# Optimization experiments

Hardware: AMD Instinct MI355X
Metric: run time of the kernel (lower is better)

The kernel has to match this reference:

```python
import math
import jax, jax.numpy as jnp
import numpy as np

B, T_IN, R = 32, 24, 512
T_HIST, WIDTH, MODES, NLAYERS = 24, 128, 64, 4
IN_CH = T_HIST + 4
STEPS = 12
DT = 1.0


def setup_inputs() -> dict:
    key = jax.random.key(0)
    ks = jax.random.split(key, 12)
    scale = 1.0 / math.sqrt(WIDTH * WIDTH)
    return {
        "z": jax.random.normal(ks[0], (B, T_IN, R), dtype=jnp.float32),
        "t_grid": jax.random.uniform(ks[1], (B, T_IN), dtype=jnp.float32) * 100.0,
        "fc0_w": jax.random.normal(ks[2], (IN_CH, WIDTH), dtype=jnp.float32) / math.sqrt(IN_CH),
        "fc0_b": jax.random.normal(ks[3], (WIDTH,), dtype=jnp.float32) * 0.01,
        "spec_wr": jax.random.normal(ks[4], (NLAYERS, WIDTH, WIDTH, MODES), dtype=jnp.float32) * scale,
        "spec_wi": jax.random.normal(ks[5], (NLAYERS, WIDTH, WIDTH, MODES), dtype=jnp.float32) * scale,
        "conv_w": jax.random.normal(ks[6], (NLAYERS, WIDTH, WIDTH), dtype=jnp.float32) / math.sqrt(WIDTH),
        "conv_b": jax.random.normal(ks[7], (NLAYERS, WIDTH), dtype=jnp.float32) * 0.01,
        "fc1_w": jax.random.normal(ks[8], (WIDTH, 2 * WIDTH), dtype=jnp.float32) / math.sqrt(WIDTH),
        "fc1_b": jax.random.normal(ks[9], (2 * WIDTH,), dtype=jnp.float32) * 0.01,
        "fc2_w": jax.random.normal(ks[10], (2 * WIDTH, 1), dtype=jnp.float32) / math.sqrt(2 * WIDTH),
        "fc2_b": jax.random.normal(ks[11], (1,), dtype=jnp.float32) * 0.01,
        "steps": STEPS,
    }


def _fno_block(h, w_cplx, cw, cb, r):
    # h: (B, W, R). Spectral conv: rfft -> truncated complex mul -> irfft.
    x_ft = jnp.fft.rfft(h, axis=-1)                      # (B, W, R//2+1) complex
    m = w_cplx.shape[-1]                                  # modes (<= R//2+1)
    out_m = jnp.einsum('bim,iom->bom', x_ft[:, :, :m], w_cplx)
    out_ft = jnp.pad(out_m, ((0, 0), (0, 0), (0, x_ft.shape[-1] - m)))
    spec = jnp.fft.irfft(out_ft, n=r, axis=-1)
    # 1x1 conv (pointwise over channels) + bias
    pw = jnp.einsum('oi,bir->bor', cw, h) + cb[None, :, None]
    return jax.nn.gelu(spec + pw, approximate=False)


def reference(z, t_grid, fc0_w, fc0_b, spec_wr, spec_wi, conv_w, conv_b,
              fc1_w, fc1_b, fc2_w, fc2_b, steps):
    b, _, r = z.shape
    t_hist = fc0_w.shape[0] - 4
    seq0 = z[:, -t_hist:]                 # (B, t_hist, R)
    t_start = t_grid[:, -1]               # (B,)
    x_coord = jnp.linspace(0.0, 1.0, r, dtype=z.dtype)  # (R,)
    spec_w = spec_wr + 1j * spec_wi       # (L, W, W, M) complex
    nlayers = conv_w.shape[0]

    def step(seq, i):
        tt = t_start + (i + 1).astype(z.dtype) * DT      # (B,)
        ang24 = 2.0 * math.pi * tt / 24.0
        ang168 = 2.0 * math.pi * tt / 168.0
        tf = jnp.stack([
            jnp.broadcast_to(jnp.sin(ang24)[:, None], (b, r)),
            jnp.broadcast_to(jnp.cos(ang24)[:, None], (b, r)),
            jnp.broadcast_to(jnp.sin(ang168)[:, None], (b, r)),
            jnp.broadcast_to(x_coord[None, :], (b, r)),
        ], axis=-1)                                       # (B, R, 4)
        h = jnp.concatenate([jnp.swapaxes(seq, 1, 2), tf], axis=-1)  # (B, R, t_hist+4)
        h = h @ fc0_w + fc0_b                             # (B, R, W)
        h = jnp.swapaxes(h, 1, 2)                         # (B, W, R)
        for l in range(nlayers):
            h = _fno_block(h, spec_w[l], conv_w[l], conv_b[l], r)
        h = jnp.swapaxes(h, 1, 2)                         # (B, R, W)
        h = jax.nn.gelu(h @ fc1_w + fc1_b, approximate=False)
        dx = (h @ fc2_w + fc2_b)[..., 0]                  # (B, R)
        z_next = seq[:, -1, :] + dx
        new_seq = jnp.concatenate([seq[:, 1:], z_next[:, None]], axis=1)
        return new_seq, z_next

    _, preds = jax.lax.scan(step, seq0, jnp.arange(steps))
    return jnp.swapaxes(preds, 0, 1)                      # (B, steps, R)
```

## Files before the change

### kernel.cpp

```cpp
#include <hip/hip_runtime.h>
#include <math.h>


#define NB 32
#define NR 512
#define NW 128
#define NM 64
#define NTH 24
#define NLAY 4
#define NSTEPS 12
#define SEQROWS 36

typedef unsigned short u16;
typedef unsigned int u32;
typedef __attribute__((ext_vector_type(8))) short bf16x8;
typedef __attribute__((ext_vector_type(4))) float f32x4;
#define MFMA16(a, b, c) __builtin_amdgcn_mfma_f32_16x16x32_bf16((a), (b), (c), 0, 0, 0)

__device__ __forceinline__ float gelu_exact(float x) {
    return 0.5f * x * (1.0f + erff(x * 0.70710678118654752f));
}
__device__ __forceinline__ float bf2f(u16 u) {
    union { u32 i; float f; } v; v.i = ((u32)u) << 16; return v.f;
}
__device__ __forceinline__ u16 f2bf_hi(float x) {
    union { float f; u32 i; } v; v.f = x; return (u16)(v.i >> 16);
}
__device__ __forceinline__ u16 f2bf_lo(float x) {
    float h = bf2f(f2bf_hi(x));
    return f2bf_hi(x - h);
}
__device__ __forceinline__ bf16x8 negbf(bf16x8 a) {
#pragma unroll
    for (int i = 0; i < 8; i++) a[i] ^= (short)0x8000;
    return a;
}

__global__ void build_tables_planes(u16* __restrict__ f1, u16* __restrict__ f2,
                                    u16* __restrict__ gt1, u16* __restrict__ gt2) {
    int idx = blockIdx.x * 256 + threadIdx.x;
    int mc = idx >> 9, r = idx & 511, m = mc & 63;
    int p = (m * r) & 511;
    float a = (float)p * (1.0f / 256.0f);
    float c = cospif(a), s = sinpif(a);
    float Fv = (mc < 64) ? c : -s;
    float cm = (m == 0) ? (1.0f / 512.0f) : (2.0f / 512.0f);
    float Gv = (mc < 64) ? cm * c : ((m == 0) ? 0.0f : -cm * s);
    f1[idx] = f2bf_hi(Fv); f2[idx] = f2bf_lo(Fv);
    size_t g = (size_t)r * 128 + mc;
    gt1[g] = f2bf_hi(Gv); gt2[g] = f2bf_lo(Gv);
}

__global__ __launch_bounds__(256) void prep_specw(const float* __restrict__ wr, const float* __restrict__ wi,
                           u16* __restrict__ wr1, u16* __restrict__ wr2,
                           u16* __restrict__ wi1, u16* __restrict__ wi2) {
    __shared__ float tile[128][65];
    int l = blockIdx.x >> 7, o = blockIdx.x & 127;
    int tid = threadIdx.x;
    size_t sbase = (size_t)l * 1048576 + (size_t)o * 64;
    size_t dbase = (size_t)l * 64 * 16384 + (size_t)o * 128;
    for (int pass = 0; pass < 2; pass++) {
        const float* src = pass ? wi : wr;
        u16* d1 = pass ? wi1 : wr1;
        u16* d2 = pass ? wi2 : wr2;
        if (pass) __syncthreads();
        for (int e = tid; e < 8192; e += 256) {
            int i = e >> 6, m = e & 63;
            tile[i][m] = src[sbase + (size_t)i * 8192 + m];
        }
        __syncthreads();
        for (int e = tid; e < 4096; e += 256) {
            int m = e >> 6, i2 = (e & 63) * 2;
            float v0 = tile[i2][m], v1 = tile[i2 + 1][m];
            u32 hh = (u32)f2bf_hi(v0) | ((u32)f2bf_hi(v1) << 16);
            u32 ll = (u32)f2bf_lo(v0) | ((u32)f2bf_lo(v1) << 16);
            size_t d = dbase + (size_t)m * 16384 + i2;
            *(u32*)&d1[d] = hh;
            *(u32*)&d2[d] = ll;
        }
    }
}

__global__ void prep_cw(const float* __restrict__ cw, u16* __restrict__ c1, u16* __restrict__ c2) {
    int idx = blockIdx.x * 256 + threadIdx.x;
    float v = cw[idx];
    c1[idx] = f2bf_hi(v); c2[idx] = f2bf_lo(v);
}

__global__ void prep_fc1t(const float* __restrict__ fc1_w,
                          u16* __restrict__ f11, u16* __restrict__ f12) {
    int idx = blockIdx.x * 256 + threadIdx.x;
    int j = idx >> 7, c = idx & 127;
    float v = fc1_w[(size_t)c * 256 + j];
    f11[idx] = f2bf_hi(v); f12[idx] = f2bf_lo(v);
}

__global__ void init_seq_kernel(const float* __restrict__ z, float* __restrict__ seq) {
    int idx = blockIdx.x * 256 + threadIdx.x;
    int b = idx / (NTH * NR);
    int rem = idx - b * (NTH * NR);
    seq[(size_t)b * SEQROWS * NR + rem] = z[idx];
}

__global__ __launch_bounds__(256) void fc0_kernel(const float* __restrict__ seq,
        const float* __restrict__ t_grid, const float* __restrict__ fc0_w,
        const float* __restrict__ fc0_b, u16* __restrict__ ht1, u16* __restrict__ ht2,
        u16* __restrict__ htc1, u16* __restrict__ htc2, int step) {
    __shared__ float wlds[28 * 128];
    __shared__ float blds[128];
    int b = blockIdx.y, rblk = blockIdx.x;
    int tid = threadIdx.x;
    for (int t = tid; t < 28 * 128; t += 256) wlds[t] = fc0_w[t];
    if (tid < 128) blds[tid] = fc0_b[tid];
    __syncthreads();
    int lane = tid & 63, wq = tid >> 6;
    int r = rblk * 64 + lane;
    float sv[24];
    const float* sp = seq + ((size_t)b * SEQROWS + step) * NR + r;
#pragma unroll
    for (int t = 0; t < 24; t++) sv[t] = sp[(size_t)t * NR];
    float tt = t_grid[b * 24 + 23] + (float)(step + 1);
    float ang24 = 6.28318530717958647692f * tt * (1.0f / 24.0f);
    float ang168 = 6.28318530717958647692f * tt * (1.0f / 168.0f);
    float s24 = sinf(ang24), c24 = cosf(ang24), s168 = sinf(ang168);
    float xc = (float)r * (1.0f / 511.0f);
    size_t rowoff = ((size_t)b * NR + r) * NW;
#pragma unroll 2
    for (int w0 = 0; w0 < 32; w0 += 2) {
        float acc2[2];
#pragma unroll
        for (int q = 0; q < 2; q++) {
            int w = wq * 32 + w0 + q;
            float acc = blds[w];
#pragma unroll
            for (int t = 0; t < 24; t++) acc += sv[t] * wlds[t * 128 + w];
            acc += s24 * wlds[24 * 128 + w] + c24 * wlds[25 * 128 + w]
                 + s168 * wlds[26 * 128 + w] + xc * wlds[27 * 128 + w];
            acc2[q] = acc;
        }
        u16 h0 = f2bf_hi(acc2[0]), h1 = f2bf_hi(acc2[1]);
        u16 l0 = f2bf_lo(acc2[0]), l1 = f2bf_lo(acc2[1]);
        size_t off = rowoff + wq * 32 + w0;
        *(u32*)&ht1[off] = (u32)h0 | ((u32)h1 << 16);
        *(u32*)&ht2[off] = (u32)l0 | ((u32)l1 << 16);
        int w = wq * 32 + w0;
        size_t coff = ((size_t)b * 128 + w) * 512 + r;
        htc1[coff] = h0; htc1[coff + 512] = h1;
        htc2[coff] = l0; htc2[coff + 512] = l1;
    }
}

__global__ __launch_bounds__(256) void dft_mfma(const u16* __restrict__ f1, const u16* __restrict__ f2,
        const u16* __restrict__ htc1, const u16* __restrict__ htc2,
        u16* __restrict__ x1, u16* __restrict__ x2) {
    __shared__ __align__(16) u16 A1[2][1280], A2[2][1280];
    __shared__ __align__(16) u16 B1[2][2560], B2[2][2560];
    int bx = blockIdx.x;
    int b = bx >> 1, ch = bx & 1;
    int mct = blockIdx.y * 32;
    int tid = threadIdx.x, wid = tid >> 6, l = tid & 63;
    int wm0 = (wid >> 1) * 16, wn0 = (wid & 1) * 32;
    int arow = (l & 15), kgrp = (l >> 4) * 8;
    f32x4 acc0 = {0.f, 0.f, 0.f, 0.f}, acc1 = {0.f, 0.f, 0.f, 0.f};
    int pa_pl = tid >> 7, pa_row = (tid >> 2) & 31, pa_seg = tid & 3;
    const u16* asrc = (pa_pl ? f2 : f1) + (size_t)(mct + pa_row) * 512 + pa_seg * 8;
    int aoff = pa_row * 40 + pa_seg * 8;
    int b_row = (tid >> 2) & 63, b_seg = tid & 3;
    const u16* bsrc1 = htc1 + ((size_t)b * 128 + ch * 64 + b_row) * 512 + b_seg * 8;
    const u16* bsrc2 = htc2 + ((size_t)b * 128 + ch * 64 + b_row) * 512 + b_seg * 8;
    int boff = b_row * 40 + b_seg * 8;
    uint4 raO, rbO0, rbO1, raE, rbE0, rbE1;
    raO = *(const uint4*)(asrc); rbO0 = *(const uint4*)(bsrc1); rbO1 = *(const uint4*)(bsrc2);
    *(uint4*)((pa_pl ? A2[0] : A1[0]) + aoff) = raO;
    *(uint4*)(B1[0] + boff) = rbO0;
    *(uint4*)(B2[0] + boff) = rbO1;
    raO = *(const uint4*)(asrc + 32); rbO0 = *(const uint4*)(bsrc1 + 32); rbO1 = *(const uint4*)(bsrc2 + 32);
    raE = *(const uint4*)(asrc + 64); rbE0 = *(const uint4*)(bsrc1 + 64); rbE1 = *(const uint4*)(bsrc2 + 64);
    __syncthreads();
#define DFT_COMPUTE(BUF)                                                       \
    {   bf16x8 a1 = *(const bf16x8*)&A1[BUF][(wm0 + arow) * 40 + kgrp];        \
        bf16x8 a2 = *(const bf16x8*)&A2[BUF][(wm0 + arow) * 40 + kgrp];        \
        bf16x8 b10 = *(const bf16x8*)&B1[BUF][(wn0 + arow) * 40 + kgrp];       \
        bf16x8 b20 = *(const bf16x8*)&B2[BUF][(wn0 + arow) * 40 + kgrp];       \
        bf16x8 b11 = *(const bf16x8*)&B1[BUF][(wn0 + 16 + arow) * 40 + kgrp];  \
        bf16x8 b21 = *(const bf16x8*)&B2[BUF][(wn0 + 16 + arow) * 40 + kgrp];  \
        acc0 = MFMA16(a1, b10, acc0);                                          \
        acc0 = MFMA16(a1, b20, acc0);                                          \
        acc0 = MFMA16(a2, b10, acc0);                                          \
        acc1 = MFMA16(a1, b11, acc1);                                          \
        acc1 = MFMA16(a1, b21, acc1);                                          \
        acc1 = MFMA16(a2, b11, acc1); }
    for (int k = 0; k < 16; k += 2) {
        DFT_COMPUTE(0)
        *(uint4*)((pa_pl ? A2[1] : A1[1]) + aoff) = raO;
        *(uint4*)(B1[1] + boff) = rbO0;
        *(uint4*)(B2[1] + boff) = rbO1;
        if (k < 13) {
            int ko = (k + 3) * 32;
            raO = *(const uint4*)(asrc + ko); rbO0 = *(const uint4*)(bsrc1 + ko); rbO1 = *(const uint4*)(bsrc2 + ko);
        }
        __syncthreads();
        DFT_COMPUTE(1)
        if (k < 14) {
            *(uint4*)((pa_pl ? A2[0] : A1[0]) + aoff) = raE;
            *(uint4*)(B1[0] + boff) = rbE0;
            *(uint4*)(B2[0] + boff) = rbE1;
            if (k < 12) {
                int ko = (k + 4) * 32;
                raE = *(const uint4*)(asrc + ko); rbE0 = *(const uint4*)(bsrc1 + ko); rbE1 = *(const uint4*)(bsrc2 + ko);
            }
        }
        __syncthreads();
    }
#undef DFT_COMPUTE
    int mcr = mct + wm0 + (l >> 4) * 4;
    int n0 = bx * 64 + wn0 + (l & 15);
#pragma unroll
    for (int j = 0; j < 4; j++) {
        size_t o0 = (size_t)(mcr + j) * 4096 + n0;
        x1[o0] = f2bf_hi(acc0[j]); x2[o0] = f2bf_lo(acc0[j]);
        size_t o1 = o0 + 16;
        x1[o1] = f2bf_hi(acc1[j]); x2[o1] = f2bf_lo(acc1[j]);
    }
}

__global__ __launch_bounds__(256) void modemix_mfma(const u16* __restrict__ x1, const u16* __restrict__ x2,
        const u16* __restrict__ wr1, const u16* __restrict__ wr2,
        const u16* __restrict__ wi1, const u16* __restrict__ wi2,
        u16* __restrict__ y1, u16* __restrict__ y2, int layer) {
    __shared__ __align__(16) u16 WR1[2][1280], WR2[2][1280], WI1[2][1280], WI2[2][1280];
    __shared__ __align__(16) u16 XR1[2][1280], XR2[2][1280], XI1[2][1280], XI2[2][1280];
    int m = blockIdx.x, oq = blockIdx.y;
    int tid = threadIdx.x, wid = tid >> 6, l = tid & 63;
    int wo0 = (wid >> 1) * 16, wb0 = (wid & 1) * 16;
    int arow = (l & 15), kgrp = (l >> 4) * 8;
    f32x4 ar = {0.f, 0.f, 0.f, 0.f}, ai = {0.f, 0.f, 0.f, 0.f};
    size_t wbase = (((size_t)layer * 64 + m) * 128 + oq * 32) * 128;
    int s0 = tid >> 7, srow = (tid >> 2) & 31, sseg = tid & 3;
    const u16* wsrc0 = (s0 ? wr2 : wr1) + wbase + (size_t)srow * 128 + sseg * 8;
    const u16* wsrc1 = (s0 ? wi2 : wi1) + wbase + (size_t)srow * 128 + sseg * 8;
    const u16* xb = s0 ? x2 : x1;
    const u16* xsrc0 = xb + (size_t)m * 4096 + srow * 128 + sseg * 8;
    const u16* xsrc1 = xb + (size_t)(64 + m) * 4096 + srow * 128 + sseg * 8;
    int soff = srow * 40 + sseg * 8;
    u16* wd0_0 = (s0 ? WR2[0] : WR1[0]) + soff;  u16* wd0_1 = (s0 ? WR2[1] : WR1[1]) + soff;
    u16* wd1_0 = (s0 ? WI2[0] : WI1[0]) + soff;  u16* wd1_1 = (s0 ? WI2[1] : WI1[1]) + soff;
    u16* xd0_0 = (s0 ? XR2[0] : XR1[0]) + soff;  u16* xd0_1 = (s0 ? XR2[1] : XR1[1]) + soff;
    u16* xd1_0 = (s0 ? XI2[0] : XI1[0]) + soff;  u16* xd1_1 = (s0 ? XI2[1] : XI1[1]) + soff;
    uint4 rwO0, rwO1, rxO0, rxO1, rwE0, rwE1, rxE0, rxE1;
    rwO0 = *(const uint4*)(wsrc0); rwO1 = *(const uint4*)(wsrc1);
    rxO0 = *(const uint4*)(xsrc0); rxO1 = *(const uint4*)(xsrc1);
    *(uint4*)wd0_0 = rwO0; *(uint4*)wd1_0 = rwO1;
    *(uint4*)xd0_0 = rxO0; *(uint4*)xd1_0 = rxO1;
    rwO0 = *(const uint4*)(wsrc0 + 32); rwO1 = *(const uint4*)(wsrc1 + 32);
    rxO0 = *(const uint4*)(xsrc0 + 32); rxO1 = *(const uint4*)(xsrc1 + 32);
    rwE0 = *(const uint4*)(wsrc0 + 64); rwE1 = *(const uint4*)(wsrc1 + 64);
    rxE0 = *(const uint4*)(xsrc0 + 64); rxE1 = *(const uint4*)(xsrc1 + 64);
    __syncthreads();
#define MM_COMPUTE(BUF)                                                        \
    {   int ao = (wo0 + arow) * 40 + kgrp;                                     \
        int bo = (wb0 + arow) * 40 + kgrp;                                     \
        bf16x8 Wr1 = *(const bf16x8*)&WR1[BUF][ao], Wr2 = *(const bf16x8*)&WR2[BUF][ao]; \
        bf16x8 Wi1 = *(const bf16x8*)&WI1[BUF][ao], Wi2 = *(const bf16x8*)&WI2[BUF][ao]; \
        bf16x8 Xr1 = *(const bf16x8*)&XR1[BUF][bo], Xr2 = *(const bf16x8*)&XR2[BUF][bo]; \
        bf16x8 Xi1 = *(const bf16x8*)&XI1[BUF][bo], Xi2 = *(const bf16x8*)&XI2[BUF][bo]; \
        bf16x8 nWi1 = negbf(Wi1), nWi2 = negbf(Wi2);                           \
        ar = MFMA16(Wr1, Xr1, ar); ar = MFMA16(Wr1, Xr2, ar); ar = MFMA16(Wr2, Xr1, ar); \
        ar = MFMA16(nWi1, Xi1, ar); ar = MFMA16(nWi1, Xi2, ar); ar = MFMA16(nWi2, Xi1, ar); \
        ai = MFMA16(Wi1, Xr1, ai); ai = MFMA16(Wi1, Xr2, ai); ai = MFMA16(Wi2, Xr1, ai); \
        ai = MFMA16(Wr1, Xi1, ai); ai = MFMA16(Wr1, Xi2, ai); ai = MFMA16(Wr2, Xi1, ai); }
    for (int k = 0; k < 4; k += 2) {
        MM_COMPUTE(0)
        *(uint4*)wd0_1 = rwO0; *(uint4*)wd1_1 = rwO1;
        *(uint4*)xd0_1 = rxO0; *(uint4*)xd1_1 = rxO1;
        if (k == 0) {
            rwO0 = *(const uint4*)(wsrc0 + 96); rwO1 = *(const uint4*)(wsrc1 + 96);
            rxO0 = *(const uint4*)(xsrc0 + 96); rxO1 = *(const uint4*)(xsrc1 + 96);
        }
        __syncthreads();
        MM_COMPUTE(1)
        if (k == 0) {
            *(uint4*)wd0_0 = rwE0; *(uint4*)wd1_0 = rwE1;
            *(uint4*)xd0_0 = rxE0; *(uint4*)xd1_0 = rxE1;
        }
        __syncthreads();
    }
#undef MM_COMPUTE
    int ob = oq * 32 + wo0 + (l >> 4) * 4;
    int bb = wb0 + (l & 15);
#pragma unroll
    for (int j = 0; j < 4; j++) {
        size_t o = ((size_t)bb * 128 + ob + j) * 128;
        y1[o + m] = f2bf_hi(ar[j]); y2[o + m] = f2bf_lo(ar[j]);
        y1[o + 64 + m] = f2bf_hi(ai[j]); y2[o + 64 + m] = f2bf_lo(ai[j]);
    }
}

__global__ __launch_bounds__(256) void idft_conv_mfma(const u16* __restrict__ y1, const u16* __restrict__ y2,
        const u16* __restrict__ gt1, const u16* __restrict__ gt2,
        const u16* __restrict__ hc1, const u16* __restrict__ hc2,
        const u16* __restrict__ cw1, const u16* __restrict__ cw2,
        const float* __restrict__ conv_b,
        u16* __restrict__ hn1, u16* __restrict__ hn2,
        u16* __restrict__ htc1, u16* __restrict__ htc2, int layer, int wtr) {
    __shared__ __align__(16) u16 A1[2][2560], A2[2][2560];
    __shared__ __align__(16) u16 B1[2][2560], B2[2][2560];
    __shared__ __align__(16) u16 T1[64 * 66], T2[64 * 66];
    int rt = blockIdx.x * 64, ot = blockIdx.y * 64, b = blockIdx.z;
    int tid = threadIdx.x, wid = tid >> 6, l = tid & 63;
    int wo0 = (wid >> 1) * 32, wr0 = (wid & 1) * 32;
    int arow = (l & 15), kgrp = (l >> 4) * 8;
    int srow = (tid >> 2) & 63, sseg = tid & 3;
    int soff = srow * 40 + sseg * 8;
    const u16* ya = y1 + ((size_t)b * 128 + ot + srow) * 128 + sseg * 8;
    const u16* yb = y2 + ((size_t)b * 128 + ot + srow) * 128 + sseg * 8;
    const u16* ca = cw1 + ((size_t)layer * 128 + ot + srow) * 128 + sseg * 8;
    const u16* cb = cw2 + ((size_t)layer * 128 + ot + srow) * 128 + sseg * 8;
    const u16* ga = gt1 + (size_t)(rt + srow) * 128 + sseg * 8;
    const u16* gb = gt2 + (size_t)(rt + srow) * 128 + sseg * 8;
    const u16* ha = hc1 + ((size_t)b * 512 + rt + srow) * 128 + sseg * 8;
    const u16* hb = hc2 + ((size_t)b * 512 + rt + srow) * 128 + sseg * 8;
    f32x4 acc[2][2] = {{{0.f,0.f,0.f,0.f},{0.f,0.f,0.f,0.f}},{{0.f,0.f,0.f,0.f},{0.f,0.f,0.f,0.f}}};
    uint4 raO0, raO1, rbO0, rbO1, raE0, raE1, rbE0, rbE1;
#define IDFT_LOAD(chk, Ra0, Ra1, Rb0, Rb1)                                    \
    {   int k0_ = ((chk) & 3) * 32;                                           \
        if ((chk) < 4) {                                                      \
            Ra0 = *(const uint4*)(ya + k0_); Ra1 = *(const uint4*)(yb + k0_); \
            Rb0 = *(const uint4*)(ga + k0_); Rb1 = *(const uint4*)(gb + k0_); \
        } else {                                                              \
            Ra0 = *(const uint4*)(ca + k0_); Ra1 = *(const uint4*)(cb + k0_); \
            Rb0 = *(const uint4*)(ha + k0_); Rb1 = *(const uint4*)(hb + k0_); \
        } }
#define IDFT_STORE(BUF, Ra0, Ra1, Rb0, Rb1)                                   \
    {   *(uint4*)(A1[BUF] + soff) = Ra0; *(uint4*)(A2[BUF] + soff) = Ra1;     \
        *(uint4*)(B1[BUF] + soff) = Rb0; *(uint4*)(B2[BUF] + soff) = Rb1; }
#define IDFT_COMPUTE(BUF)                                                     \
    {   bf16x8 bfr[2][2];                                                     \
        _Pragma("unroll")                                                     \
        for (int rf = 0; rf < 2; rf++) {                                      \
            bfr[rf][0] = *(const bf16x8*)&B1[BUF][(wr0 + rf * 16 + arow) * 40 + kgrp]; \
            bfr[rf][1] = *(const bf16x8*)&B2[BUF][(wr0 + rf * 16 + arow) * 40 + kgrp]; \
        }                                                                     \
        _Pragma("unroll")                                                     \
        for (int of = 0; of < 2; of++) {                                      \
            bf16x8 a1 = *(const bf16x8*)&A1[BUF][(wo0 + of * 16 + arow) * 40 + kgrp]; \
            bf16x8 a2 = *(const bf16x8*)&A2[BUF][(wo0 + of * 16 + arow) * 40 + kgrp]; \
            _Pragma("unroll")                                                 \
            for (int rf = 0; rf < 2; rf++) {                                  \
                acc[of][rf] = MFMA16(a1, bfr[rf][0], acc[of][rf]);            \
                acc[of][rf] = MFMA16(a1, bfr[rf][1], acc[of][rf]);            \
                acc[of][rf] = MFMA16(a2, bfr[rf][0], acc[of][rf]);            \
            }                                                                 \
        } }
    IDFT_LOAD(0, raO0, raO1, rbO0, rbO1)
    IDFT_STORE(0, raO0, raO1, rbO0, rbO1)
    IDFT_LOAD(1, raO0, raO1, rbO0, rbO1)
    IDFT_LOAD(2, raE0, raE1, rbE0, rbE1)
    __syncthreads();
    for (int k = 0; k < 8; k += 2) {
        IDFT_COMPUTE(0)
        IDFT_STORE(1, raO0, raO1, rbO0, rbO1)
        if (k < 5) IDFT_LOAD(k + 3, raO0, raO1, rbO0, rbO1)
        __syncthreads();
        IDFT_COMPUTE(1)
        if (k < 6) {
            IDFT_STORE(0, raE0, raE1, rbE0, rbE1)
            if (k < 4) IDFT_LOAD(k + 4, raE0, raE1, rbE0, rbE1)
        }
        __syncthreads();
    }
#undef IDFT_LOAD
#undef IDFT_STORE
#undef IDFT_COMPUTE
#pragma unroll
    for (int of = 0; of < 2; of++) {
        int obl = wo0 + of * 16 + (l >> 4) * 4;
        int ob = ot + obl;
#pragma unroll
        for (int rf = 0; rf < 2; rf++) {
            int rloc = wr0 + rf * 16 + (l & 15);
            int r = rt + rloc;
            float v0 = gelu_exact(acc[of][rf][0] + conv_b[layer * 128 + ob + 0]);
            float v1 = gelu_exact(acc[of][rf][1] + conv_b[layer * 128 + ob + 1]);
            float v2 = gelu_exact(acc[of][rf][2] + conv_b[layer * 128 + ob + 2]);
            float v3 = gelu_exact(acc[of][rf][3] + conv_b[layer * 128 + ob + 3]);
            ushort4 hv, lv;
            hv.x = f2bf_hi(v0); hv.y = f2bf_hi(v1); hv.z = f2bf_hi(v2); hv.w = f2bf_hi(v3);
            lv.x = f2bf_lo(v0); lv.y = f2bf_lo(v1); lv.z = f2bf_lo(v2); lv.w = f2bf_lo(v3);
            size_t off = ((size_t)b * 512 + r) * 128 + ob;
            *(ushort4*)&hn1[off] = hv;
            *(ushort4*)&hn2[off] = lv;
            if (wtr) {
                T1[(obl + 0) * 66 + rloc] = hv.x; T1[(obl + 1) * 66 + rloc] = hv.y;
                T1[(obl + 2) * 66 + rloc] = hv.z; T1[(obl + 3) * 66 + rloc] = hv.w;
                T2[(obl + 0) * 66 + rloc] = lv.x; T2[(obl + 1) * 66 + rloc] = lv.y;
                T2[(obl + 2) * 66 + rloc] = lv.z; T2[(obl + 3) * 66 + rloc] = lv.w;
            }
        }
    }
    if (wtr) {
        __syncthreads();
#pragma unroll
        for (int q = 0; q < 8; q++) {
            int t = tid + q * 256;
            int o = t >> 5, ru = t & 31;
            u32 vh = *(const u32*)&T1[o * 66 + ru * 2];
            u32 vl = *(const u32*)&T2[o * 66 + ru * 2];
            size_t off = ((size_t)b * 128 + ot + o) * 512 + rt + ru * 2;
            *(u32*)&htc1[off] = vh;
            *(u32*)&htc2[off] = vl;
        }
    }
}

__global__ __launch_bounds__(256) void head_mfma(const u16* __restrict__ ht1, const u16* __restrict__ ht2,
        const u16* __restrict__ f11, const u16* __restrict__ f12,
        const float* __restrict__ fc1_b, const float* __restrict__ fc2_w,
        const float* __restrict__ fc2_b,
        const float* __restrict__ t_grid, const float* __restrict__ fc0_w,
        const float* __restrict__ fc0_b,
        float* __restrict__ seq, float* __restrict__ preds,
        u16* __restrict__ nht1, u16* __restrict__ nht2,
        u16* __restrict__ nhtc1, u16* __restrict__ nhtc2,
        int step, int do_fc0) {
    __shared__ __align__(16) u16 POOL[25600];
    __shared__ float fc2s[256], fc1bs[256];
    u16* HA1 = POOL;
    u16* HA2 = POOL + 10240;
    u16* HB1 = POOL + 20480;
    u16* HB2 = POOL + 23040;
    int blk = blockIdx.x;
    int b = blk >> 3, r0 = (blk & 7) * 64;
    int tid = threadIdx.x, wid = tid >> 6, l = tid & 63;
    fc2s[tid] = fc2_w[tid];
    fc1bs[tid] = fc1_b[tid];
    int arow = l & 15, kgrp = (l >> 4) * 8;
    f32x4 acc[16];
#pragma unroll
    for (int jf = 0; jf < 16; jf++) acc[jf] = (f32x4){0.f, 0.f, 0.f, 0.f};
    for (int k0 = 0; k0 < 128; k0 += 32) {
        __syncthreads();
#pragma unroll
        for (int q = 0; q < 8; q++) {
            int t = tid + q * 256;
            int pl = t >> 10, j = (t >> 2) & 255, seg = t & 3;
            const u16* src = (pl ? f12 : f11) + (size_t)j * 128 + k0 + seg * 8;
            *(uint4*)((pl ? HA2 : HA1) + j * 40 + seg * 8) = *(const uint4*)src;
        }
#pragma unroll
        for (int q = 0; q < 2; q++) {
            int t = tid + q * 256;
            int pl = t >> 8, rr = (t >> 2) & 63, seg = t & 3;
            const u16* src = (pl ? ht2 : ht1) + ((size_t)b * 512 + r0 + rr) * 128 + k0 + seg * 8;
            *(uint4*)((pl ? HB2 : HB1) + rr * 40 + seg * 8) = *(const uint4*)src;
        }
        __syncthreads();
        int bo = (wid * 16 + arow) * 40 + kgrp;
        bf16x8 b1 = *(const bf16x8*)&HB1[bo];
        bf16x8 b2 = *(const bf16x8*)&HB2[bo];
#pragma unroll
        for (int jf = 0; jf < 16; jf++) {
            int ao = (jf * 16 + arow) * 40 + kgrp;
            bf16x8 a1 = *(const bf16x8*)&HA1[ao];
            bf16x8 a2 = *(const bf16x8*)&HA2[ao];
            acc[jf] = MFMA16(a1, b1, acc[jf]);
            acc[jf] = MFMA16(a1, b2, acc[jf]);
            acc[jf] = MFMA16(a2, b1, acc[jf]);
        }
    }
    __syncthreads();
    float dx = 0.0f;
#pragma unroll
    for (int jf = 0; jf < 16; jf++) {
        int jbase = jf * 16 + (l >> 4) * 4;
#pragma unroll
        for (int jj = 0; jj < 4; jj++) {
            int j = jbase + jj;
            dx += gelu_exact(acc[jf][jj] + fc1bs[j]) * fc2s[j];
        }
    }
    dx += __shfl_xor(dx, 16);
    dx += __shfl_xor(dx, 32);
    bool zlane = ((l >> 4) == 0);
    int rml = wid * 16 + arow;
    float zn = 0.0f;
    if (zlane) {
        int r = r0 + rml;
        zn = seq[((size_t)b * SEQROWS + step + 23) * NR + r] + dx + fc2_b[0];
        seq[((size_t)b * SEQROWS + step + 24) * NR + r] = zn;
        preds[((size_t)b * NSTEPS + step) * NR + r] = zn;
    }
    if (!do_fc0) return;
    float* win = (float*)POOL;
    float* wl  = (float*)POOL + 2048;
    float* bl  = (float*)POOL + 2048 + 3584;
    for (int t = tid; t < 23 * 64; t += 256) {
        int tr = t >> 6, c = t & 63;
        win[tr * 64 + c] = seq[((size_t)b * SEQROWS + step + 1 + tr) * NR + r0 + c];
    }
    for (int t = tid; t < 28 * 128; t += 256) wl[t] = fc0_w[t];
    if (tid < 128) bl[tid] = fc0_b[tid];
    if (zlane) win[23 * 64 + rml] = zn;
    __syncthreads();
    int lane = tid & 63, wq = tid >> 6;
    int r = r0 + lane;
    float sv[24];
#pragma unroll
    for (int t = 0; t < 24; t++) sv[t] = win[t * 64 + lane];
    float tt = t_grid[b * 24 + 23] + (float)(step + 2);
    float ang24 = 6.28318530717958647692f * tt * (1.0f / 24.0f);
    float ang168 = 6.28318530717958647692f * tt * (1.0f / 168.0f);
    float s24 = sinf(ang24), c24 = cosf(ang24), s168 = sinf(ang168);
    float xc = (float)r * (1.0f / 511.0f);
    size_t rowoff = ((size_t)b * NR + r) * NW;
#pragma unroll 2
    for (int w0 = 0; w0 < 32; w0 += 2) {
        float acc2[2];
#pragma unroll
        for (int q = 0; q < 2; q++) {
            int w = wq * 32 + w0 + q;
            float a = bl[w];
#pragma unroll
            for (int t = 0; t < 24; t++) a += sv[t] * wl[t * 128 + w];
            a += s24 * wl[24 * 128 + w] + c24 * wl[25 * 128 + w]
               + s168 * wl[26 * 128 + w] + xc * wl[27 * 128 + w];
            acc2[q] = a;
        }
        u16 h0 = f2bf_hi(acc2[0]), h1 = f2bf_hi(acc2[1]);
        u16 l0 = f2bf_lo(acc2[0]), l1 = f2bf_lo(acc2[1]);
        size_t off = rowoff + wq * 32 + w0;
        *(u32*)&nht1[off] = (u32)h0 | ((u32)h1 << 16);
        *(u32*)&nht2[off] = (u32)l0 | ((u32)l1 << 16);
        int w = wq * 32 + w0;
        size_t coff = ((size_t)b * 128 + w) * 512 + r;
        nhtc1[coff] = h0; nhtc1[coff + 512] = h1;
        nhtc2[coff] = l0; nhtc2[coff + 512] = l1;
    }
}

extern "C" void kernel_launch(void* const* d_in, const int* in_sizes, int n_in,
                              void* d_out, int out_size, void* d_ws, size_t ws_size,
                              hipStream_t stream) {
    (void)in_sizes; (void)n_in; (void)out_size; (void)ws_size;
    const float* z       = (const float*)d_in[0];
    const float* t_grid  = (const float*)d_in[1];
    const float* fc0_w   = (const float*)d_in[2];
    const float* fc0_b   = (const float*)d_in[3];
    const float* spec_wr = (const float*)d_in[4];
    const float* spec_wi = (const float*)d_in[5];
    const float* conv_w  = (const float*)d_in[6];
    const float* conv_b  = (const float*)d_in[7];
    const float* fc1_w   = (const float*)d_in[8];
    const float* fc1_b   = (const float*)d_in[9];
    const float* fc2_w   = (const float*)d_in[10];
    const float* fc2_b   = (const float*)d_in[11];
    float* preds = (float*)d_out;

    char* p = (char*)d_ws;
    float* seq = (float*)p;  p += (size_t)NB * SEQROWS * NR * 4;
    u16* ht1 = (u16*)p;  p += (size_t)2 * NB * NR * NW * 2;
    u16* ht2 = (u16*)p;  p += (size_t)2 * NB * NR * NW * 2;
    u16* htc1 = (u16*)p; p += (size_t)NB * NW * NR * 2;
    u16* htc2 = (u16*)p; p += (size_t)NB * NW * NR * 2;
    u16* x1  = (u16*)p;  p += (size_t)128 * 4096 * 2;
    u16* x2  = (u16*)p;  p += (size_t)128 * 4096 * 2;
    u16* y1  = (u16*)p;  p += (size_t)NB * NW * 128 * 2;
    u16* y2  = (u16*)p;  p += (size_t)NB * NW * 128 * 2;
    u16* f1  = (u16*)p;  p += (size_t)128 * 512 * 2;
    u16* f2  = (u16*)p;  p += (size_t)128 * 512 * 2;
    u16* gt1 = (u16*)p;  p += (size_t)512 * 128 * 2;
    u16* gt2 = (u16*)p;  p += (size_t)512 * 128 * 2;
    u16* wr1 = (u16*)p;  p += (size_t)NLAY * NM * NW * NW * 2;
    u16* wr2 = (u16*)p;  p += (size_t)NLAY * NM * NW * NW * 2;
    u16* wi1 = (u16*)p;  p += (size_t)NLAY * NM * NW * NW * 2;
    u16* wi2 = (u16*)p;  p += (size_t)NLAY * NM * NW * NW * 2;
    u16* cw1 = (u16*)p;  p += (size_t)NLAY * NW * NW * 2;
    u16* cw2 = (u16*)p;  p += (size_t)NLAY * NW * NW * 2;
    u16* f11 = (u16*)p;  p += (size_t)256 * 128 * 2;
    u16* f12 = (u16*)p;  p += (size_t)256 * 128 * 2;

    const size_t htplane = (size_t)NB * NR * NW;

    build_tables_planes<<<256, 256, 0, stream>>>(f1, f2, gt1, gt2);
    prep_specw<<<512, 256, 0, stream>>>(spec_wr, spec_wi, wr1, wr2, wi1, wi2);
    prep_cw<<<256, 256, 0, stream>>>(conv_w, cw1, cw2);
    prep_fc1t<<<128, 256, 0, stream>>>(fc1_w, f11, f12);
    init_seq_kernel<<<(NB * NTH * NR) / 256, 256, 0, stream>>>(z, seq);

    for (int step = 0; step < NSTEPS; step++) {
        if (step == 0) {
            fc0_kernel<<<dim3(8, 32), 256, 0, stream>>>(seq, t_grid, fc0_w, fc0_b,
                                                        ht1, ht2, htc1, htc2, step);
        }
        int cur = 0;
        for (int l = 0; l < NLAY; l++) {
            const u16* hc1 = ht1 + (size_t)cur * htplane;
            const u16* hc2 = ht2 + (size_t)cur * htplane;
            u16* hn1 = ht1 + (size_t)(cur ^ 1) * htplane;
            u16* hn2 = ht2 + (size_t)(cur ^ 1) * htplane;
            dft_mfma<<<dim3(64, 4), 256, 0, stream>>>(f1, f2, htc1, htc2, x1, x2);
            modemix_mfma<<<dim3(64, 4), 256, 0, stream>>>(x1, x2, wr1, wr2, wi1, wi2,
                                                          y1, y2, l);
            idft_conv_mfma<<<dim3(8, 2, 32), 256, 0, stream>>>(y1, y2, gt1, gt2,
                                                               hc1, hc2, cw1, cw2,
                                                               conv_b, hn1, hn2,
                                                               htc1, htc2, l, (l < 3) ? 1 : 0);
            cur ^= 1;
        }
        head_mfma<<<256, 256, 0, stream>>>(ht1, ht2, f11, f12, fc1_b, fc2_w, fc2_b,
                                           t_grid, fc0_w, fc0_b, seq, preds,
                                           ht1, ht2, htc1, htc2,
                                           step, (step < NSTEPS - 1) ? 1 : 0);
    }
}
```

Before: 1.807 ms.

## Retile DFT GEMM for more blocks and load modemix operands in one pass

The DFT kernel now gives each block a 32x32 output tile instead of 32x64, doubling the grid to 128x4 blocks. It also uses a 64-wide K chunk per stage, so each wave runs one accumulator with more MFMAs per barrier. The modemix kernel drops its double-buffered pipeline and loads all eight 32x128 slabs into one shared pool up front, followed by a single barrier and an unrolled MFMA loop. The goal is more parallelism and fewer syncs in the spectral stages, at the cost of more shared memory per modemix block, which can lower occupancy, and no overlap of loads with compute.

```diff
diff --git a/kernel.cpp b/kernel.cpp
--- a/kernel.cpp
+++ b/kernel.cpp
@@ -153,74 +153,71 @@
 __global__ __launch_bounds__(256) void dft_mfma(const u16* __restrict__ f1, const u16* __restrict__ f2,
         const u16* __restrict__ htc1, const u16* __restrict__ htc2,
         u16* __restrict__ x1, u16* __restrict__ x2) {
-    __shared__ __align__(16) u16 A1[2][1280], A2[2][1280];
-    __shared__ __align__(16) u16 B1[2][2560], B2[2][2560];
+    __shared__ __align__(16) u16 A1[2][32 * 72], A2[2][32 * 72];
+    __shared__ __align__(16) u16 B1[2][32 * 72], B2[2][32 * 72];
     int bx = blockIdx.x;
-    int b = bx >> 1, ch = bx & 1;
     int mct = blockIdx.y * 32;
     int tid = threadIdx.x, wid = tid >> 6, l = tid & 63;
-    int wm0 = (wid >> 1) * 16, wn0 = (wid & 1) * 32;
-    int arow = (l & 15), kgrp = (l >> 4) * 8;
-    f32x4 acc0 = {0.f, 0.f, 0.f, 0.f}, acc1 = {0.f, 0.f, 0.f, 0.f};
-    int pa_pl = tid >> 7, pa_row = (tid >> 2) & 31, pa_seg = tid & 3;
-    const u16* asrc = (pa_pl ? f2 : f1) + (size_t)(mct + pa_row) * 512 + pa_seg * 8;
-    int aoff = pa_row * 40 + pa_seg * 8;
-    int b_row = (tid >> 2) & 63, b_seg = tid & 3;
-    const u16* bsrc1 = htc1 + ((size_t)b * 128 + ch * 64 + b_row) * 512 + b_seg * 8;
-    const u16* bsrc2 = htc2 + ((size_t)b * 128 + ch * 64 + b_row) * 512 + b_seg * 8;
-    int boff = b_row * 40 + b_seg * 8;
-    uint4 raO, rbO0, rbO1, raE, rbE0, rbE1;
-    raO = *(const uint4*)(asrc); rbO0 = *(const uint4*)(bsrc1); rbO1 = *(const uint4*)(bsrc2);
-    *(uint4*)((pa_pl ? A2[0] : A1[0]) + aoff) = raO;
-    *(uint4*)(B1[0] + boff) = rbO0;
-    *(uint4*)(B2[0] + boff) = rbO1;
-    raO = *(const uint4*)(asrc + 32); rbO0 = *(const uint4*)(bsrc1 + 32); rbO1 = *(const uint4*)(bsrc2 + 32);
-    raE = *(const uint4*)(asrc + 64); rbE0 = *(const uint4*)(bsrc1 + 64); rbE1 = *(const uint4*)(bsrc2 + 64);
+    int wm0 = (wid >> 1) * 16, wn0 = (wid & 1) * 16;
+    int arow = l & 15, kgrp = (l >> 4) * 8;
+    f32x4 acc = {0.f, 0.f, 0.f, 0.f};
+    int pl = tid >> 7, row = (tid >> 2) & 31, sp = (tid & 3) * 16;
+    const u16* asrc = (pl ? f2 : f1) + (size_t)(mct + row) * 512 + sp;
+    const u16* bsrc = (pl ? htc2 : htc1)
+                      + ((size_t)(bx >> 2) * 128 + (bx & 3) * 32 + row) * 512 + sp;
+    int loff = row * 72 + sp;
+    u16* ad0 = (pl ? A2[0] : A1[0]) + loff;  u16* ad1 = (pl ? A2[1] : A1[1]) + loff;
+    u16* bd0 = (pl ? B2[0] : B1[0]) + loff;  u16* bd1 = (pl ? B2[1] : B1[1]) + loff;
+    uint4 oA0, oA1, oB0, oB1, eA0, eA1, eB0, eB1;
+    oA0 = *(const uint4*)(asrc);     oA1 = *(const uint4*)(asrc + 8);
+    oB0 = *(const uint4*)(bsrc);     oB1 = *(const uint4*)(bsrc + 8);
+    *(uint4*)ad0 = oA0; *(uint4*)(ad0 + 8) = oA1;
+    *(uint4*)bd0 = oB0; *(uint4*)(bd0 + 8) = oB1;
+    oA0 = *(const uint4*)(asrc + 64);  oA1 = *(const uint4*)(asrc + 72);
+    oB0 = *(const uint4*)(bsrc + 64);  oB1 = *(const uint4*)(bsrc + 72);
+    eA0 = *(const uint4*)(asrc + 128); eA1 = *(const uint4*)(asrc + 136);
+    eB0 = *(const uint4*)(bsrc + 128); eB1 = *(const uint4*)(bsrc + 136);
     __syncthreads();
 #define DFT_COMPUTE(BUF)                                                       \
-    {   bf16x8 a1 = *(const bf16x8*)&A1[BUF][(wm0 + arow) * 40 + kgrp];        \
-        bf16x8 a2 = *(const bf16x8*)&A2[BUF][(wm0 + arow) * 40 + kgrp];        \
-        bf16x8 b10 = *(const bf16x8*)&B1[BUF][(wn0 + arow) * 40 + kgrp];       \
-        bf16x8 b20 = *(const bf16x8*)&B2[BUF][(wn0 + arow) * 40 + kgrp];       \
-        bf16x8 b11 = *(const bf16x8*)&B1[BUF][(wn0 + 16 + arow) * 40 + kgrp];  \
-        bf16x8 b21 = *(const bf16x8*)&B2[BUF][(wn0 + 16 + arow) * 40 + kgrp];  \
-        acc0 = MFMA16(a1, b10, acc0);                                          \
-        acc0 = MFMA16(a1, b20, acc0);                                          \
-        acc0 = MFMA16(a2, b10, acc0);                                          \
-        acc1 = MFMA16(a1, b11, acc1);                                          \
-        acc1 = MFMA16(a1, b21, acc1);                                          \
-        acc1 = MFMA16(a2, b11, acc1); }
-    for (int k = 0; k < 16; k += 2) {
+    { _Pragma("unroll")                                                        \
+      for (int kk = 0; kk < 64; kk += 32) {                                    \
+        bf16x8 a1 = *(const bf16x8*)&A1[BUF][(wm0 + arow) * 72 + kk + kgrp];   \
+        bf16x8 a2 = *(const bf16x8*)&A2[BUF][(wm0 + arow) * 72 + kk + kgrp];   \
+        bf16x8 b1 = *(const bf16x8*)&B1[BUF][(wn0 + arow) * 72 + kk + kgrp];   \
+        bf16x8 b2 = *(const bf16x8*)&B2[BUF][(wn0 + arow) * 72 + kk + kgrp];   \
+        acc = MFMA16(a1, b1, acc);                                             \
+        acc = MFMA16(a1, b2, acc);                                             \
+        acc = MFMA16(a2, b1, acc);                                             \
+      } }
+    for (int k = 0; k < 8; k += 2) {
         DFT_COMPUTE(0)
-        *(uint4*)((pa_pl ? A2[1] : A1[1]) + aoff) = raO;
-        *(uint4*)(B1[1] + boff) = rbO0;
-        *(uint4*)(B2[1] + boff) = rbO1;
-        if (k < 13) {
-            int ko = (k + 3) * 32;
-            raO = *(const uint4*)(asrc + ko); rbO0 = *(const uint4*)(bsrc1 + ko); rbO1 = *(const uint4*)(bsrc2 + ko);
+        *(uint4*)ad1 = oA0; *(uint4*)(ad1 + 8) = oA1;
+        *(uint4*)bd1 = oB0; *(uint4*)(bd1 + 8) = oB1;
+        if (k < 5) {
+            int ko = (k + 3) * 64;
+            oA0 = *(const uint4*)(asrc + ko);      oA1 = *(const uint4*)(asrc + ko + 8);
+            oB0 = *(const uint4*)(bsrc + ko);      oB1 = *(const uint4*)(bsrc + ko + 8);
         }
         __syncthreads();
         DFT_COMPUTE(1)
-        if (k < 14) {
-            *(uint4*)((pa_pl ? A2[0] : A1[0]) + aoff) = raE;
-            *(uint4*)(B1[0] + boff) = rbE0;
-            *(uint4*)(B2[0] + boff) = rbE1;
-            if (k < 12) {
-                int ko = (k + 4) * 32;
-                raE = *(const uint4*)(asrc + ko); rbE0 = *(const uint4*)(bsrc1 + ko); rbE1 = *(const uint4*)(bsrc2 + ko);
+        if (k < 6) {
+            *(uint4*)ad0 = eA0; *(uint4*)(ad0 + 8) = eA1;
+            *(uint4*)bd0 = eB0; *(uint4*)(bd0 + 8) = eB1;
+            if (k < 4) {
+                int ko = (k + 4) * 64;
+                eA0 = *(const uint4*)(asrc + ko);  eA1 = *(const uint4*)(asrc + ko + 8);
+                eB0 = *(const uint4*)(bsrc + ko);  eB1 = *(const uint4*)(bsrc + ko + 8);
             }
         }
         __syncthreads();
     }
 #undef DFT_COMPUTE
     int mcr = mct + wm0 + (l >> 4) * 4;
-    int n0 = bx * 64 + wn0 + (l & 15);
+    int n0 = bx * 32 + wn0 + (l & 15);
 #pragma unroll
     for (int j = 0; j < 4; j++) {
         size_t o0 = (size_t)(mcr + j) * 4096 + n0;
-        x1[o0] = f2bf_hi(acc0[j]); x2[o0] = f2bf_lo(acc0[j]);
-        size_t o1 = o0 + 16;
-        x1[o1] = f2bf_hi(acc1[j]); x2[o1] = f2bf_lo(acc1[j]);
+        x1[o0] = f2bf_hi(acc[j]); x2[o0] = f2bf_lo(acc[j]);
     }
 }
 
@@ -228,64 +225,50 @@
         const u16* __restrict__ wr1, const u16* __restrict__ wr2,
         const u16* __restrict__ wi1, const u16* __restrict__ wi2,
         u16* __restrict__ y1, u16* __restrict__ y2, int layer) {
-    __shared__ __align__(16) u16 WR1[2][1280], WR2[2][1280], WI1[2][1280], WI2[2][1280];
-    __shared__ __align__(16) u16 XR1[2][1280], XR2[2][1280], XI1[2][1280], XI2[2][1280];
+    __shared__ __align__(16) u16 POOL[8 * 32 * 136];
     int m = blockIdx.x, oq = blockIdx.y;
     int tid = threadIdx.x, wid = tid >> 6, l = tid & 63;
     int wo0 = (wid >> 1) * 16, wb0 = (wid & 1) * 16;
-    int arow = (l & 15), kgrp = (l >> 4) * 8;
+    int arow = l & 15, kgrp = (l >> 4) * 8;
+    size_t wbase = (((size_t)layer * 64 + m) * 128 + oq * 32) * 128;
+#pragma unroll
+    for (int q = 0; q < 16; q++) {
+        const int slab = q >> 1;
+        int rr = ((q & 1) << 4) + (tid >> 4);
+        int seg = tid & 15;
+        const u16* src;
+        if      (slab == 0) src = wr1 + wbase + (size_t)rr * 128 + seg * 8;
+        else if (slab == 1) src = wr2 + wbase + (size_t)rr * 128 + seg * 8;
+        else if (slab == 2) src = wi1 + wbase + (size_t)rr * 128 + seg * 8;
+        else if (slab == 3) src = wi2 + wbase + (size_t)rr * 128 + seg * 8;
+        else if (slab == 4) src = x1 + (size_t)m * 4096 + rr * 128 + seg * 8;
+        else if (slab == 5) src = x2 + (size_t)m * 4096 + rr * 128 + seg * 8;
+        else if (slab == 6) src = x1 + (size_t)(64 + m) * 4096 + rr * 128 + seg * 8;
+        else                src = x2 + (size_t)(64 + m) * 4096 + rr * 128 + seg * 8;
+        *(uint4*)&POOL[slab * 4352 + rr * 136 + seg * 8] = *(const uint4*)src;
+    }
+    __syncthreads();
     f32x4 ar = {0.f, 0.f, 0.f, 0.f}, ai = {0.f, 0.f, 0.f, 0.f};
-    size_t wbase = (((size_t)layer * 64 + m) * 128 + oq * 32) * 128;
-    int s0 = tid >> 7, srow = (tid >> 2) & 31, sseg = tid & 3;
-    const u16* wsrc0 = (s0 ? wr2 : wr1) + wbase + (size_t)srow * 128 + sseg * 8;
-    const u16* wsrc1 = (s0 ? wi2 : wi1) + wbase + (size_t)srow * 128 + sseg * 8;
-    const u16* xb = s0 ? x2 : x1;
-    const u16* xsrc0 = xb + (size_t)m * 4096 + srow * 128 + sseg * 8;
-    const u16* xsrc1 = xb + (size_t)(64 + m) * 4096 + srow * 128 + sseg * 8;
-    int soff = srow * 40 + sseg * 8;
-    u16* wd0_0 = (s0 ? WR2[0] : WR1[0]) + soff;  u16* wd0_1 = (s0 ? WR2[1] : WR1[1]) + soff;
-    u16* wd1_0 = (s0 ? WI2[0] : WI1[0]) + soff;  u16* wd1_1 = (s0 ? WI2[1] : WI1[1]) + soff;
-    u16* xd0_0 = (s0 ? XR2[0] : XR1[0]) + soff;  u16* xd0_1 = (s0 ? XR2[1] : XR1[1]) + soff;
-    u16* xd1_0 = (s0 ? XI2[0] : XI1[0]) + soff;  u16* xd1_1 = (s0 ? XI2[1] : XI1[1]) + soff;
-    uint4 rwO0, rwO1, rxO0, rxO1, rwE0, rwE1, rxE0, rxE1;
-    rwO0 = *(const uint4*)(wsrc0); rwO1 = *(const uint4*)(wsrc1);
-    rxO0 = *(const uint4*)(xsrc0); rxO1 = *(const uint4*)(xsrc1);
-    *(uint4*)wd0_0 = rwO0; *(uint4*)wd1_0 = rwO1;
-    *(uint4*)xd0_0 = rxO0; *(uint4*)xd1_0 = rxO1;
-    rwO0 = *(const uint4*)(wsrc0 + 32); rwO1 = *(const uint4*)(wsrc1 + 32);
-    rxO0 = *(const uint4*)(xsrc0 + 32); rxO1 = *(const uint4*)(xsrc1 + 32);
-    rwE0 = *(const uint4*)(wsrc0 + 64); rwE1 = *(const uint4*)(wsrc1 + 64);
-    rxE0 = *(const uint4*)(xsrc0 + 64); rxE1 = *(const uint4*)(xsrc1 + 64);
-    __syncthreads();
-#define MM_COMPUTE(BUF)                                                        \
-    {   int ao = (wo0 + arow) * 40 + kgrp;                                     \
-        int bo = (wb0 + arow) * 40 + kgrp;                                     \
-        bf16x8 Wr1 = *(const bf16x8*)&WR1[BUF][ao], Wr2 = *(const bf16x8*)&WR2[BUF][ao]; \
-        bf16x8 Wi1 = *(const bf16x8*)&WI1[BUF][ao], Wi2 = *(const bf16x8*)&WI2[BUF][ao]; \
-        bf16x8 Xr1 = *(const bf16x8*)&XR1[BUF][bo], Xr2 = *(const bf16x8*)&XR2[BUF][bo]; \
-        bf16x8 Xi1 = *(const bf16x8*)&XI1[BUF][bo], Xi2 = *(const bf16x8*)&XI2[BUF][bo]; \
-        bf16x8 nWi1 = negbf(Wi1), nWi2 = negbf(Wi2);                           \
-        ar = MFMA16(Wr1, Xr1, ar); ar = MFMA16(Wr1, Xr2, ar); ar = MFMA16(Wr2, Xr1, ar); \
-        ar = MFMA16(nWi1, Xi1, ar); ar = MFMA16(nWi1, Xi2, ar); ar = MFMA16(nWi2, Xi1, ar); \
-        ai = MFMA16(Wi1, Xr1, ai); ai = MFMA16(Wi1, Xr2, ai); ai = MFMA16(Wi2, Xr1, ai); \
-        ai = MFMA16(Wr1, Xi1, ai); ai = MFMA16(Wr1, Xi2, ai); ai = MFMA16(Wr2, Xi1, ai); }
-    for (int k = 0; k < 4; k += 2) {
-        MM_COMPUTE(0)
-        *(uint4*)wd0_1 = rwO0; *(uint4*)wd1_1 = rwO1;
-        *(uint4*)xd0_1 = rxO0; *(uint4*)xd1_1 = rxO1;
-        if (k == 0) {
-            rwO0 = *(const uint4*)(wsrc0 + 96); rwO1 = *(const uint4*)(wsrc1 + 96);
-            rxO0 = *(const uint4*)(xsrc0 + 96); rxO1 = *(const uint4*)(xsrc1 + 96);
-        }
-        __syncthreads();
-        MM_COMPUTE(1)
-        if (k == 0) {
-            *(uint4*)wd0_0 = rwE0; *(uint4*)wd1_0 = rwE1;
-            *(uint4*)xd0_0 = rxE0; *(uint4*)xd1_0 = rxE1;
-        }
-        __syncthreads();
-    }
-#undef MM_COMPUTE
+    int aoB = (wo0 + arow) * 136 + kgrp;
+    int boB = (wb0 + arow) * 136 + kgrp;
+#pragma unroll
+    for (int kg = 0; kg < 4; kg++) {
+        int ao = aoB + kg * 32;
+        int bo = boB + kg * 32;
+        bf16x8 Wr1 = *(const bf16x8*)&POOL[0 * 4352 + ao];
+        bf16x8 Wr2 = *(const bf16x8*)&POOL[1 * 4352 + ao];
+        bf16x8 Wi1 = *(const bf16x8*)&POOL[2 * 4352 + ao];
+        bf16x8 Wi2 = *(const bf16x8*)&POOL[3 * 4352 + ao];
+        bf16x8 Xr1 = *(const bf16x8*)&POOL[4 * 4352 + bo];
+        bf16x8 Xr2 = *(const bf16x8*)&POOL[5 * 4352 + bo];
+        bf16x8 Xi1 = *(const bf16x8*)&POOL[6 * 4352 + bo];
+        bf16x8 Xi2 = *(const bf16x8*)&POOL[7 * 4352 + bo];
+        bf16x8 nWi1 = negbf(Wi1), nWi2 = negbf(Wi2);
+        ar = MFMA16(Wr1, Xr1, ar); ar = MFMA16(Wr1, Xr2, ar); ar = MFMA16(Wr2, Xr1, ar);
+        ar = MFMA16(nWi1, Xi1, ar); ar = MFMA16(nWi1, Xi2, ar); ar = MFMA16(nWi2, Xi1, ar);
+        ai = MFMA16(Wi1, Xr1, ai); ai = MFMA16(Wi1, Xr2, ai); ai = MFMA16(Wi2, Xr1, ai);
+        ai = MFMA16(Wr1, Xi1, ai); ai = MFMA16(Wr1, Xi2, ai); ai = MFMA16(Wr2, Xi1, ai);
+    }
     int ob = oq * 32 + wo0 + (l >> 4) * 4;
     int bb = wb0 + (l & 15);
 #pragma unroll
@@ -598,7 +581,7 @@
             const u16* hc2 = ht2 + (size_t)cur * htplane;
             u16* hn1 = ht1 + (size_t)(cur ^ 1) * htplane;
             u16* hn2 = ht2 + (size_t)(cur ^ 1) * htplane;
-            dft_mfma<<<dim3(64, 4), 256, 0, stream>>>(f1, f2, htc1, htc2, x1, x2);
+            dft_mfma<<<dim3(128, 4), 256, 0, stream>>>(f1, f2, htc1, htc2, x1, x2);
             modemix_mfma<<<dim3(64, 4), 256, 0, stream>>>(x1, x2, wr1, wr2, wi1, wi2,
                                                           y1, y2, l);
             idft_conv_mfma<<<dim3(8, 2, 32), 256, 0, stream>>>(y1, y2, gt1, gt2,
```

Result: no change. 1.810 ms (median of 2 runs) (+0.2%).
